# Performance work log

Measured on AMD Instinct MI355X. Metric: run time of the kernel, lower is better.

## Reference

```python
import jax, jax.numpy as jnp
import numpy as np

ENC_DIM, DEC_DIM, HID_DIM = 512, 1024, 128
B, T = 64, 2048


def setup_inputs() -> dict:
    key = jax.random.key(0)
    ks = jax.random.split(key, 8)
    encoder_outs = jax.random.normal(ks[0], (B, T, ENC_DIM), dtype=jnp.float32)
    decoder_state = jax.random.normal(ks[1], (B, DEC_DIM), dtype=jnp.float32)
    mask = jax.random.randint(ks[2], (B, T), 0, 2) == 1
    # parameters (torch nn.Linear: y = x @ W.T + b)
    sV = 1.0 / np.sqrt(ENC_DIM)
    sW = 1.0 / np.sqrt(DEC_DIM)
    sw = 1.0 / np.sqrt(HID_DIM)
    V_w = jax.random.uniform(ks[3], (HID_DIM, ENC_DIM), minval=-sV, maxval=sV)
    V_b = jax.random.uniform(ks[4], (HID_DIM,), minval=-sV, maxval=sV)
    W_w = jax.random.uniform(ks[5], (HID_DIM, DEC_DIM), minval=-sW, maxval=sW)
    w_w = jax.random.uniform(ks[6], (1, HID_DIM), minval=-sw, maxval=sw)
    w_b = jax.random.uniform(ks[7], (1,), minval=-sw, maxval=sw)
    return {"encoder_outs": encoder_outs, "decoder_state": decoder_state,
            "mask": mask, "V_w": V_w, "V_b": V_b, "W_w": W_w,
            "w_w": w_w, "w_b": w_b}


def reference(encoder_outs, decoder_state, mask, V_w, V_b, W_w, w_w, w_b):
    # [B,1,H] query projection + [B,T,H] key projection
    q = jnp.einsum('bd,hd->bh', decoder_state, W_w)[:, None, :]
    k = jnp.einsum('bte,he->bth', encoder_outs, V_w) + V_b
    # scores: [B,T]
    erg = jnp.einsum('bth,h->bt', jnp.tanh(q + k), w_w[0]) + w_b[0]
    erg = jnp.where(mask, -jnp.inf, erg)
    attention_weights = jax.nn.softmax(erg, axis=1)
    attention_context = jnp.einsum('bte,bt->be', encoder_outs, attention_weights)
    return (attention_context, attention_weights)
```

## Files before the change

kernel.cpp:

```cpp
#include <hip/hip_runtime.h>
#include <hip/hip_bf16.h>

#define Bn   64
#define Tn   2048
#define ENCD 512
#define DECD 1024
#define HIDD 128
#define TT   32
#define NCH  (Tn / TT)
#define LROW 520

typedef __attribute__((ext_vector_type(8))) short bf16x8;
typedef __attribute__((ext_vector_type(4))) float f32x4;

__device__ __forceinline__ unsigned short f2bf(float f) {
    union { float f; unsigned u; } v; v.f = f;
    unsigned r = v.u + 0x7FFFu + ((v.u >> 16) & 1u);
    return (unsigned short)(r >> 16);
}
__device__ __forceinline__ float bf2f(unsigned short s) {
    union { unsigned u; float f; } v; v.u = ((unsigned)s) << 16;
    return v.f;
}
__device__ __forceinline__ float tanh_fast(float x) {
    float xa = fminf(fmaxf(x, -10.f), 10.f);
    float e = __expf(2.f * xa);
    return (e - 1.f) / (e + 1.f);
}

__global__ __launch_bounds__(128) void prep(
    const float* __restrict__ dec, const float* __restrict__ Ww,
    const float* __restrict__ Vb,  const float* __restrict__ Vw,
    float* __restrict__ qb, unsigned short* __restrict__ Vbf)
{
    int blk = blockIdx.x, tid = threadIdx.x;
    if (blk < Bn) {
        int b = blk, h = tid;
        const float4* w = (const float4*)(Ww + (size_t)h * DECD);
        const float4* d = (const float4*)(dec + (size_t)b * DECD);
        float acc = Vb[h];
        #pragma unroll 4
        for (int i = 0; i < DECD / 4; ++i) {
            float4 a = d[i], bb = w[i];
            acc += a.x * bb.x + a.y * bb.y + a.z * bb.z + a.w * bb.w;
        }
        qb[b * HIDD + h] = acc;
    } else {
        int c = blk - Bn;
        int base = c * 1024;
        #pragma unroll
        for (int i = 0; i < 8; ++i) {
            int idx = base + i * 128 + tid;
            Vbf[idx] = f2bf(Vw[idx]);
        }
    }
}

__global__ __launch_bounds__(256) void attn_main(
    const float* __restrict__ enc, const int* __restrict__ mask,
    const float* __restrict__ qb,  const unsigned short* __restrict__ Vbf,
    const float* __restrict__ ww,  const float* __restrict__ wb,
    float* __restrict__ pW, float* __restrict__ mC, float* __restrict__ lC,
    float* __restrict__ ctxP)
{
    __shared__ unsigned short encS[TT * LROW];
    __shared__ float sS[TT * HIDD];
    __shared__ float ergS[TT];
    __shared__ float pS[TT];

    const int chunk = blockIdx.x, b = blockIdx.y;
    const int tid = threadIdx.x;
    const int t0 = chunk * TT;

    const float* encTile = enc + ((size_t)b * Tn + t0) * ENCD;
    #pragma unroll
    for (int it = 0; it < 16; ++it) {
        int f4 = it * 256 + tid;
        float4 v = ((const float4*)encTile)[f4];
        int elem = f4 * 4;
        int t = elem >> 9, e = elem & 511;
        ushort4 u;
        u.x = f2bf(v.x); u.y = f2bf(v.y); u.z = f2bf(v.z); u.w = f2bf(v.w);
        *(ushort4*)&encS[t * LROW + e] = u;
    }
    __syncthreads();

    const int wave = tid >> 6, lane = tid & 63;
    const int li = lane & 15, quad = lane >> 4;

    f32x4 acc[2][2];
    #pragma unroll
    for (int mt = 0; mt < 2; ++mt)
        #pragma unroll
        for (int nt = 0; nt < 2; ++nt)
            acc[mt][nt] = (f32x4){0.f, 0.f, 0.f, 0.f};

    const unsigned short* vrow0 = Vbf + (size_t)(wave * 32 + 0  + li) * ENCD;
    const unsigned short* vrow1 = Vbf + (size_t)(wave * 32 + 16 + li) * ENCD;

    #pragma unroll 4
    for (int ks = 0; ks < 16; ++ks) {
        int k0 = ks * 32 + quad * 8;
        bf16x8 a0 = *(const bf16x8*)&encS[(0  + li) * LROW + k0];
        bf16x8 a1 = *(const bf16x8*)&encS[(16 + li) * LROW + k0];
        bf16x8 b0 = *(const bf16x8*)(vrow0 + k0);
        bf16x8 b1 = *(const bf16x8*)(vrow1 + k0);
        acc[0][0] = __builtin_amdgcn_mfma_f32_16x16x32_bf16(a0, b0, acc[0][0], 0, 0, 0);
        acc[0][1] = __builtin_amdgcn_mfma_f32_16x16x32_bf16(a0, b1, acc[0][1], 0, 0, 0);
        acc[1][0] = __builtin_amdgcn_mfma_f32_16x16x32_bf16(a1, b0, acc[1][0], 0, 0, 0);
        acc[1][1] = __builtin_amdgcn_mfma_f32_16x16x32_bf16(a1, b1, acc[1][1], 0, 0, 0);
    }

    float qv[2], wv[2];
    #pragma unroll
    for (int nt = 0; nt < 2; ++nt) {
        int h = wave * 32 + nt * 16 + li;
        qv[nt] = qb[b * HIDD + h];
        wv[nt] = ww[h];
    }
    #pragma unroll
    for (int mt = 0; mt < 2; ++mt)
        #pragma unroll
        for (int nt = 0; nt < 2; ++nt)
            #pragma unroll
            for (int r = 0; r < 4; ++r) {
                float x = acc[mt][nt][r] + qv[nt];
                float s = tanh_fast(x) * wv[nt];
                int t = mt * 16 + quad * 4 + r;
                sS[t * HIDD + wave * 32 + nt * 16 + li] = s;
            }
    __syncthreads();

    {
        int t = tid >> 3, seg = tid & 7;
        const float* row = &sS[t * HIDD + seg * 16];
        float part = 0.f;
        #pragma unroll
        for (int j = 0; j < 16; ++j) part += row[j];
        part += __shfl_xor(part, 1);
        part += __shfl_xor(part, 2);
        part += __shfl_xor(part, 4);
        if (seg == 0) {
            float e = part + wb[0];
            if (mask[b * Tn + t0 + t] != 0) e = -INFINITY;
            ergS[t] = e;
        }
    }
    __syncthreads();

    if (wave == 0) {
        float e = (lane < TT) ? ergS[lane] : -INFINITY;
        float m = e;
        #pragma unroll
        for (int off = 32; off >= 1; off >>= 1)
            m = fmaxf(m, __shfl_xor(m, off));
        float p = (e == -INFINITY) ? 0.f : __expf(e - m);
        float l = p;
        #pragma unroll
        for (int off = 32; off >= 1; off >>= 1)
            l += __shfl_xor(l, off);
        if (lane < TT) {
            pS[lane] = p;
            pW[(size_t)b * Tn + t0 + lane] = p;
        }
        if (lane == 0) {
            mC[b * NCH + chunk] = m;
            lC[b * NCH + chunk] = l;
        }
    }
    __syncthreads();

    {
        int e0 = tid * 2;
        float c0 = 0.f, c1 = 0.f;
        #pragma unroll 8
        for (int t = 0; t < TT; ++t) {
            float pt = pS[t];
            unsigned pk = *(const unsigned*)&encS[t * LROW + e0];
            c0 += pt * bf2f((unsigned short)(pk & 0xffff));
            c1 += pt * bf2f((unsigned short)(pk >> 16));
        }
        float2 cv; cv.x = c0; cv.y = c1;
        *(float2*)&ctxP[((size_t)(b * NCH + chunk)) * ENCD + e0] = cv;
    }
}

__global__ __launch_bounds__(256) void finalize(
    const float* __restrict__ mC, const float* __restrict__ lC,
    const float* __restrict__ pW, const float* __restrict__ ctxP,
    float* __restrict__ out)
{
    __shared__ float scaleS[NCH];
    __shared__ float invLs;
    const int b = blockIdx.x, tid = threadIdx.x;
    const int wave = tid >> 6, lane = tid & 63;

    if (wave == 0) {
        float m = mC[b * NCH + lane];
        float l = lC[b * NCH + lane];
        float gm = m;
        #pragma unroll
        for (int off = 32; off >= 1; off >>= 1)
            gm = fmaxf(gm, __shfl_xor(gm, off));
        float sc = (m == -INFINITY) ? 0.f : __expf(m - gm);
        float ls = l * sc;
        #pragma unroll
        for (int off = 32; off >= 1; off >>= 1)
            ls += __shfl_xor(ls, off);
        scaleS[lane] = sc;
        if (lane == 0) invLs = 1.f / ls;
    }
    __syncthreads();
    const float invL = invLs;

    float* outw = out + Bn * ENCD;
    for (int t = tid; t < Tn; t += 256)
        outw[(size_t)b * Tn + t] = pW[(size_t)b * Tn + t] * scaleS[t >> 5] * invL;

    int e0 = tid * 2;
    float c0 = 0.f, c1 = 0.f;
    for (int c = 0; c < NCH; ++c) {
        float sc = scaleS[c];
        float2 v = *(const float2*)&ctxP[((size_t)(b * NCH + c)) * ENCD + e0];
        c0 += sc * v.x;
        c1 += sc * v.y;
    }
    out[b * ENCD + e0]     = c0 * invL;
    out[b * ENCD + e0 + 1] = c1 * invL;
}

extern "C" void kernel_launch(void* const* d_in, const int* in_sizes, int n_in,
                              void* d_out, int out_size, void* d_ws, size_t ws_size,
                              hipStream_t stream)
{
    const float* enc  = (const float*)d_in[0];
    const float* dec  = (const float*)d_in[1];
    const int*   mask = (const int*)d_in[2];
    const float* Vw   = (const float*)d_in[3];
    const float* Vb   = (const float*)d_in[4];
    const float* Ww   = (const float*)d_in[5];
    const float* ww   = (const float*)d_in[6];
    const float* wb   = (const float*)d_in[7];
    float* out = (float*)d_out;
    float* ws  = (float*)d_ws;

    float*          qb   = ws;
    unsigned short* Vbf  = (unsigned short*)(ws + 8192);
    float*          pW   = ws + 40960;
    float*          mC   = ws + 172032;
    float*          lC   = ws + 176128;
    float*          ctxP = ws + 180224;

    hipLaunchKernelGGL(prep, dim3(128), dim3(128), 0, stream, dec, Ww, Vb, Vw, qb, Vbf);
    hipLaunchKernelGGL(attn_main, dim3(NCH, Bn), dim3(256), 0, stream,
                       enc, mask, qb, Vbf, ww, wb, pW, mC, lC, ctxP);
    hipLaunchKernelGGL(finalize, dim3(Bn), dim3(256), 0, stream, mC, lC, pW, ctxP, out);
}
```

Baseline: 463.4 us.

## Widen attention blocks to 512 threads and split prep/finalize across more blocks

Result: faster. 390.8 us (-15.7%).

```diff
diff --git a/kernel.cpp b/kernel.cpp
--- a/kernel.cpp
+++ b/kernel.cpp
@@ -28,35 +28,45 @@
     return (e - 1.f) / (e + 1.f);
 }
 
-__global__ __launch_bounds__(128) void prep(
+__global__ __launch_bounds__(256) void prep(
     const float* __restrict__ dec, const float* __restrict__ Ww,
     const float* __restrict__ Vb,  const float* __restrict__ Vw,
     float* __restrict__ qb, unsigned short* __restrict__ Vbf)
 {
-    int blk = blockIdx.x, tid = threadIdx.x;
-    if (blk < Bn) {
-        int b = blk, h = tid;
+    const int blk = blockIdx.x, tid = threadIdx.x;
+    if (blk < 512) {
+        const int b = blk >> 3, hg = blk & 7;
+        const int h_local = tid >> 4, seg = tid & 15;
+        const int h = hg * 16 + h_local;
         const float4* w = (const float4*)(Ww + (size_t)h * DECD);
         const float4* d = (const float4*)(dec + (size_t)b * DECD);
-        float acc = Vb[h];
-        #pragma unroll 4
-        for (int i = 0; i < DECD / 4; ++i) {
-            float4 a = d[i], bb = w[i];
+        float acc = 0.f;
+        #pragma unroll
+        for (int j = 0; j < 16; ++j) {
+            int f4 = j * 16 + seg;
+            float4 a = d[f4], bb = w[f4];
             acc += a.x * bb.x + a.y * bb.y + a.z * bb.z + a.w * bb.w;
         }
-        qb[b * HIDD + h] = acc;
+        acc += __shfl_xor(acc, 1);
+        acc += __shfl_xor(acc, 2);
+        acc += __shfl_xor(acc, 4);
+        acc += __shfl_xor(acc, 8);
+        if (seg == 0) qb[b * HIDD + h] = acc + Vb[h];
     } else {
-        int c = blk - Bn;
-        int base = c * 1024;
-        #pragma unroll
-        for (int i = 0; i < 8; ++i) {
-            int idx = base + i * 128 + tid;
-            Vbf[idx] = f2bf(Vw[idx]);
-        }
-    }
-}
-
-__global__ __launch_bounds__(256) void attn_main(
+        const int c = blk - 512;
+        const float4* src = (const float4*)Vw;
+        #pragma unroll
+        for (int i = 0; i < 2; ++i) {
+            int f4 = c * 512 + tid * 2 + i;
+            float4 v = src[f4];
+            ushort4 u;
+            u.x = f2bf(v.x); u.y = f2bf(v.y); u.z = f2bf(v.z); u.w = f2bf(v.w);
+            *(ushort4*)&Vbf[f4 * 4] = u;
+        }
+    }
+}
+
+__global__ __launch_bounds__(512, 8) void attn_main(
     const float* __restrict__ enc, const int* __restrict__ mask,
     const float* __restrict__ qb,  const unsigned short* __restrict__ Vbf,
     const float* __restrict__ ww,  const float* __restrict__ wb,
@@ -64,92 +74,74 @@
     float* __restrict__ ctxP)
 {
     __shared__ unsigned short encS[TT * LROW];
-    __shared__ float sS[TT * HIDD];
-    __shared__ float ergS[TT];
+    __shared__ float wpart[8][TT];
     __shared__ float pS[TT];
 
     const int chunk = blockIdx.x, b = blockIdx.y;
     const int tid = threadIdx.x;
     const int t0 = chunk * TT;
-
-    const float* encTile = enc + ((size_t)b * Tn + t0) * ENCD;
-    #pragma unroll
-    for (int it = 0; it < 16; ++it) {
-        int f4 = it * 256 + tid;
-        float4 v = ((const float4*)encTile)[f4];
-        int elem = f4 * 4;
-        int t = elem >> 9, e = elem & 511;
-        ushort4 u;
-        u.x = f2bf(v.x); u.y = f2bf(v.y); u.z = f2bf(v.z); u.w = f2bf(v.w);
-        *(ushort4*)&encS[t * LROW + e] = u;
-    }
-    __syncthreads();
-
     const int wave = tid >> 6, lane = tid & 63;
     const int li = lane & 15, quad = lane >> 4;
 
-    f32x4 acc[2][2];
-    #pragma unroll
-    for (int mt = 0; mt < 2; ++mt)
-        #pragma unroll
-        for (int nt = 0; nt < 2; ++nt)
-            acc[mt][nt] = (f32x4){0.f, 0.f, 0.f, 0.f};
-
-    const unsigned short* vrow0 = Vbf + (size_t)(wave * 32 + 0  + li) * ENCD;
-    const unsigned short* vrow1 = Vbf + (size_t)(wave * 32 + 16 + li) * ENCD;
+    const int h = wave * 16 + li;
+    const float qv = qb[b * HIDD + h];
+    const float wv = ww[h];
+
+    const float* encTile = enc + ((size_t)b * Tn + t0) * ENCD;
+    {
+        float4 v[8];
+        #pragma unroll
+        for (int it = 0; it < 8; ++it)
+            v[it] = ((const float4*)encTile)[it * 512 + tid];
+        #pragma unroll
+        for (int it = 0; it < 8; ++it) {
+            int f4 = it * 512 + tid;
+            int t = f4 >> 7, e = (f4 & 127) * 4;
+            ushort4 u;
+            u.x = f2bf(v[it].x); u.y = f2bf(v[it].y);
+            u.z = f2bf(v[it].z); u.w = f2bf(v[it].w);
+            *(ushort4*)&encS[t * LROW + e] = u;
+        }
+    }
+    __syncthreads();
+
+    f32x4 acc[2];
+    acc[0] = (f32x4){0.f, 0.f, 0.f, 0.f};
+    acc[1] = (f32x4){0.f, 0.f, 0.f, 0.f};
+    const unsigned short* vrow = Vbf + (size_t)h * ENCD;
 
     #pragma unroll 4
     for (int ks = 0; ks < 16; ++ks) {
         int k0 = ks * 32 + quad * 8;
         bf16x8 a0 = *(const bf16x8*)&encS[(0  + li) * LROW + k0];
         bf16x8 a1 = *(const bf16x8*)&encS[(16 + li) * LROW + k0];
-        bf16x8 b0 = *(const bf16x8*)(vrow0 + k0);
-        bf16x8 b1 = *(const bf16x8*)(vrow1 + k0);
-        acc[0][0] = __builtin_amdgcn_mfma_f32_16x16x32_bf16(a0, b0, acc[0][0], 0, 0, 0);
-        acc[0][1] = __builtin_amdgcn_mfma_f32_16x16x32_bf16(a0, b1, acc[0][1], 0, 0, 0);
-        acc[1][0] = __builtin_amdgcn_mfma_f32_16x16x32_bf16(a1, b0, acc[1][0], 0, 0, 0);
-        acc[1][1] = __builtin_amdgcn_mfma_f32_16x16x32_bf16(a1, b1, acc[1][1], 0, 0, 0);
-    }
-
-    float qv[2], wv[2];
-    #pragma unroll
-    for (int nt = 0; nt < 2; ++nt) {
-        int h = wave * 32 + nt * 16 + li;
-        qv[nt] = qb[b * HIDD + h];
-        wv[nt] = ww[h];
-    }
+        bf16x8 bb = *(const bf16x8*)(vrow + k0);
+        acc[0] = __builtin_amdgcn_mfma_f32_16x16x32_bf16(a0, bb, acc[0], 0, 0, 0);
+        acc[1] = __builtin_amdgcn_mfma_f32_16x16x32_bf16(a1, bb, acc[1], 0, 0, 0);
+    }
+
     #pragma unroll
     for (int mt = 0; mt < 2; ++mt)
         #pragma unroll
-        for (int nt = 0; nt < 2; ++nt)
+        for (int r = 0; r < 4; ++r) {
+            float s = tanh_fast(acc[mt][r] + qv) * wv;
+            s += __shfl_xor(s, 1);
+            s += __shfl_xor(s, 2);
+            s += __shfl_xor(s, 4);
+            s += __shfl_xor(s, 8);
+            if (li == 0) wpart[wave][mt * 16 + quad * 4 + r] = s;
+        }
+    __syncthreads();
+
+    if (wave == 0) {
+        float e = -INFINITY;
+        if (lane < TT) {
+            int t = lane;
+            float v = wb[0];
             #pragma unroll
-            for (int r = 0; r < 4; ++r) {
-                float x = acc[mt][nt][r] + qv[nt];
-                float s = tanh_fast(x) * wv[nt];
-                int t = mt * 16 + quad * 4 + r;
-                sS[t * HIDD + wave * 32 + nt * 16 + li] = s;
-            }
-    __syncthreads();
-
-    {
-        int t = tid >> 3, seg = tid & 7;
-        const float* row = &sS[t * HIDD + seg * 16];
-        float part = 0.f;
-        #pragma unroll
-        for (int j = 0; j < 16; ++j) part += row[j];
-        part += __shfl_xor(part, 1);
-        part += __shfl_xor(part, 2);
-        part += __shfl_xor(part, 4);
-        if (seg == 0) {
-            float e = part + wb[0];
-            if (mask[b * Tn + t0 + t] != 0) e = -INFINITY;
-            ergS[t] = e;
-        }
-    }
-    __syncthreads();
-
-    if (wave == 0) {
-        float e = (lane < TT) ? ergS[lane] : -INFINITY;
+            for (int w = 0; w < 8; ++w) v += wpart[w][t];
+            e = (mask[b * Tn + t0 + t] != 0) ? -INFINITY : v;
+        }
         float m = e;
         #pragma unroll
         for (int off = 32; off >= 1; off >>= 1)
@@ -171,17 +163,11 @@
     __syncthreads();
 
     {
-        int e0 = tid * 2;
-        float c0 = 0.f, c1 = 0.f;
+        float c = 0.f;
         #pragma unroll 8
-        for (int t = 0; t < TT; ++t) {
-            float pt = pS[t];
-            unsigned pk = *(const unsigned*)&encS[t * LROW + e0];
-            c0 += pt * bf2f((unsigned short)(pk & 0xffff));
-            c1 += pt * bf2f((unsigned short)(pk >> 16));
-        }
-        float2 cv; cv.x = c0; cv.y = c1;
-        *(float2*)&ctxP[((size_t)(b * NCH + chunk)) * ENCD + e0] = cv;
+        for (int t = 0; t < TT; ++t)
+            c += pS[t] * bf2f(encS[t * LROW + tid]);
+        ctxP[((size_t)(b * NCH + chunk)) * ENCD + tid] = c;
     }
 }
 
@@ -192,7 +178,8 @@
 {
     __shared__ float scaleS[NCH];
     __shared__ float invLs;
-    const int b = blockIdx.x, tid = threadIdx.x;
+    __shared__ float red[256];
+    const int b = blockIdx.x, part = blockIdx.y, tid = threadIdx.x;
     const int wave = tid >> 6, lane = tid & 63;
 
     if (wave == 0) {
@@ -213,20 +200,27 @@
     __syncthreads();
     const float invL = invLs;
 
-    float* outw = out + Bn * ENCD;
-    for (int t = tid; t < Tn; t += 256)
-        outw[(size_t)b * Tn + t] = pW[(size_t)b * Tn + t] * scaleS[t >> 5] * invL;
-
-    int e0 = tid * 2;
-    float c0 = 0.f, c1 = 0.f;
-    for (int c = 0; c < NCH; ++c) {
-        float sc = scaleS[c];
-        float2 v = *(const float2*)&ctxP[((size_t)(b * NCH + c)) * ENCD + e0];
-        c0 += sc * v.x;
-        c1 += sc * v.y;
-    }
-    out[b * ENCD + e0]     = c0 * invL;
-    out[b * ENCD + e0 + 1] = c1 * invL;
+    if (part < 4) {
+        const int e = part * 128 + (tid & 127);
+        const int half = tid >> 7;
+        float c = 0.f;
+        #pragma unroll 8
+        for (int cc = half * 32; cc < half * 32 + 32; ++cc)
+            c += scaleS[cc] * ctxP[((size_t)(b * NCH + cc)) * ENCD + e];
+        red[tid] = c;
+        __syncthreads();
+        if (tid < 128) {
+            int ee = part * 128 + tid;
+            out[b * ENCD + ee] = (red[tid] + red[tid + 128]) * invL;
+        }
+    } else {
+        float* outw = out + Bn * ENCD;
+        #pragma unroll
+        for (int i = 0; i < 8; ++i) {
+            int t = i * 256 + tid;
+            outw[(size_t)b * Tn + t] = pW[(size_t)b * Tn + t] * scaleS[t >> 5] * invL;
+        }
+    }
 }
 
 extern "C" void kernel_launch(void* const* d_in, const int* in_sizes, int n_in,
@@ -251,8 +245,8 @@
     float*          lC   = ws + 176128;
     float*          ctxP = ws + 180224;
 
-    hipLaunchKernelGGL(prep, dim3(128), dim3(128), 0, stream, dec, Ww, Vb, Vw, qb, Vbf);
-    hipLaunchKernelGGL(attn_main, dim3(NCH, Bn), dim3(256), 0, stream,
+    hipLaunchKernelGGL(prep, dim3(576), dim3(256), 0, stream, dec, Ww, Vb, Vw, qb, Vbf);
+    hipLaunchKernelGGL(attn_main, dim3(NCH, Bn), dim3(512), 0, stream,
                        enc, mask, qb, Vbf, ww, wb, pW, mC, lC, ctxP);
-    hipLaunchKernelGGL(finalize, dim3(Bn), dim3(256), 0, stream, mC, lC, pW, ctxP, out);
-}
+    hipLaunchKernelGGL(finalize, dim3(Bn, 5), dim3(256), 0, stream, mC, lC, pW, ctxP, out);
+}
```
